# Optimization experiments

Hardware: AMD Instinct MI355X
Metric: run time of the kernel (lower is better)

Reference implementation:

```python
import jax, jax.numpy as jnp
import numpy as np

EPS = 0.01
EXPD_WEIGHT = 1.0
COMP_WEIGHT = 1.0
NUM_CLASSES = 32
M, D = 262144, 128


def setup_inputs() -> dict:
    key = jax.random.key(0)
    k1, k2 = jax.random.split(key)
    cls_score = jax.random.normal(k1, (M, D), dtype=jnp.float32)
    label = jax.random.randint(k2, (M,), 0, NUM_CLASSES)
    return {"cls_score": cls_score, "label": label}


def _logdet(X):
    sgn, ld = jnp.linalg.slogdet(X)
    return sgn * ld


def reference(cls_score, label):
    m, d = cls_score.shape
    m_f = jnp.asarray(m, cls_score.dtype)
    # expansion term: logdet(c * Z^T Z) / 2, c = d / (m * eps)
    c = d / (m_f * EPS)
    cov = cls_score.T @ cls_score  # [d, d]
    loss_expd = _logdet(c * cov) / 2.0

    # compression term: sum_j m_j/(2m) * logdet(c_j * Z_j^T Z_j)
    def per_class(j):
        mask = (label == j).astype(cls_score.dtype)  # [m]
        m_j = mask.sum()
        safe_mj = jnp.maximum(m_j, 1.0)
        c_j = d / (safe_mj * EPS)
        # Z_j^T Z_j == (mask * Z)^T Z, honoring the boolean subset without gather
        cov_j = (cls_score * mask[:, None]).T @ cls_score  # [d, d]
        ld_j = _logdet(c_j * cov_j)
        return jnp.where(m_j > 0, ld_j * m_j / (2.0 * m_f), 0.0)

    comps = jax.lax.map(per_class, jnp.arange(NUM_CLASSES))  # [J]
    loss_comp = comps.sum()

    # MCR2Loss.forward with return_all=False
    return loss_comp * COMP_WEIGHT - loss_expd * EXPD_WEIGHT
```

## Files before the change

### kernel.cpp

```cpp
#include <hip/hip_runtime.h>
#include <math.h>

#define D 128
#define NCLS 32
#define TSLOT 16
#define CHUNK 256

typedef float f32x16 __attribute__((ext_vector_type(16)));
typedef short bf16x8 __attribute__((ext_vector_type(8)));

__global__ void zero_k(int* hist) {
  int t = threadIdx.x;
  if (t < NCLS) hist[t] = 0;
}

__global__ __launch_bounds__(64) void hist_blk_k(const int* __restrict__ label, int M,
                                                 int NB, int* __restrict__ blkhist_t,
                                                 int* __restrict__ hist) {
  __shared__ int h[NCLS];
  const int lane = threadIdx.x;
  const int b = blockIdx.x;
  if (lane < NCLS) h[lane] = 0;
  __syncthreads();
  const int s0 = b * CHUNK;
#pragma unroll
  for (int it = 0; it < CHUNK / 64; ++it) {
    int i = s0 + it * 64 + lane;
    if (i < M) atomicAdd(&h[label[i]], 1);
  }
  __syncthreads();
  if (lane < NCLS) {
    blkhist_t[lane * NB + b] = h[lane];
    atomicAdd(&hist[lane], h[lane]);
  }
}

__global__ void prefix_k(const int* __restrict__ hist, int* __restrict__ cstart) {
  if (threadIdx.x == 0) {
    int run = 0;
    for (int j = 0; j < NCLS; ++j) { cstart[j] = run; run += hist[j]; }
    cstart[NCLS] = run;
  }
}

__global__ __launch_bounds__(64) void base_k(const int* __restrict__ blkhist_t,
                                             const int* __restrict__ cstart, int NB,
                                             int* __restrict__ base_t) {
  const int j = blockIdx.x;
  const int lane = threadIdx.x;
  const int K = (NB + 63) / 64;
  int vals[32];
  int run = 0;
  for (int k = 0; k < K; ++k) {
    int b = lane * K + k;
    int v = (b < NB) ? blkhist_t[j * NB + b] : 0;
    vals[k] = v;
    run += v;
  }
  int incl = run;
  for (int off = 1; off < 64; off <<= 1) {
    int o = __shfl_up(incl, off);
    if (lane >= off) incl += o;
  }
  int pos = cstart[j] + (incl - run);
  for (int k = 0; k < K; ++k) {
    int b = lane * K + k;
    if (b < NB) base_t[j * NB + b] = pos;
    pos += vals[k];
  }
}

__global__ __launch_bounds__(64) void scatter2_k(const int* __restrict__ label, int M,
                                                 int NB, const int* __restrict__ base_t,
                                                 int* __restrict__ idxbuf) {
  __shared__ int cur[NCLS];
  const int b = blockIdx.x;
  const int lane = threadIdx.x;
  if (lane < NCLS) cur[lane] = base_t[lane * NB + b];
  __syncthreads();
  const int s0 = b * CHUNK;
#pragma unroll
  for (int it = 0; it < CHUNK / 64; ++it) {
    int i = s0 + it * 64 + lane;
    int j = (i < M) ? label[i] : -1;
    unsigned long long mask = 0;
#pragma unroll
    for (int q = 0; q < NCLS; ++q) {
      unsigned long long mm = __ballot(j == q);
      if (j == q) mask = mm;
    }
    if (j >= 0) {
      int myoff = __popcll(mask & ((1ull << lane) - 1ull));
      int basec = cur[j];
      idxbuf[basec + myoff] = i;
      if (myoff == 0) cur[j] = basec + __popcll(mask);
    }
    __syncthreads();
  }
}

__device__ inline void bsplit(float x, short& hi, short& lo) {
  unsigned u = __float_as_uint(x);
  unsigned rh = u + 0x7fffu + ((u >> 16) & 1u);
  unsigned short h = (unsigned short)(rh >> 16);
  float hf = __uint_as_float((unsigned)h << 16);
  float l = x - hf;
  unsigned ul = __float_as_uint(l);
  unsigned rl = ul + 0x7fffu + ((ul >> 16) & 1u);
  hi = (short)h;
  lo = (short)(rl >> 16);
}

__global__ __launch_bounds__(512, 4) void cov_k(const float* __restrict__ Z,
                                                const int* __restrict__ idxbuf,
                                                const int* __restrict__ hist,
                                                const int* __restrict__ cstart,
                                                float* __restrict__ partials) {
  __shared__ __attribute__((aligned(16))) char arena[2 * 16896];
  char* const ThiB = arena;
  char* const TloB = arena + 16896;

  const int b = blockIdx.x;
  const int cls = b / TSLOT, slot = b % TSLOT;
  const int t = threadIdx.x;
  const int lane = t & 63;
  const int w = t >> 6;
  const int r = w >> 1;
  const int cp = (w & 1) * 2;

  const int col4 = t & 31;
  const int rg = t >> 5;
  const int wbase0 = (((rg >> 2) * 4 + (col4 >> 3)) * 2 + ((rg >> 1) & 1)) * 528 +
                     (col4 & 7) * 16 + (rg & 1) * 8;

  const int mj = hist[cls];
  const int seg0 = cstart[cls];
  const int segend = seg0 + mj;
  const int nch = (mj + 63) / 64;

  f32x16 acc[2];
#pragma unroll
  for (int u = 0; u < 2; ++u)
#pragma unroll
    for (int i = 0; i < 16; ++i) acc[u][i] = 0.f;

  const int n = lane & 31;
  const int poff = ((n >> 2) + 8 * (n & 3)) * 16 + (lane >> 5) * 528;

  float4 pv[4];
  {
    const int ch = slot;
    const int r0 = seg0 + ch * 64;
#pragma unroll
    for (int i = 0; i < 4; ++i) {
      int gr = r0 + rg * 4 + i;
      if (ch < nch && gr < segend) {
        int ridx = idxbuf[gr];
        pv[i] = *(const float4*)(Z + (size_t)ridx * D + col4 * 4);
      } else {
        pv[i] = make_float4(0.f, 0.f, 0.f, 0.f);
      }
    }
  }

  for (int ch = slot; ch < nch; ch += TSLOT) {
    __syncthreads();
    {
      float xs[4][4];
      xs[0][0] = pv[0].x; xs[0][1] = pv[0].y; xs[0][2] = pv[0].z; xs[0][3] = pv[0].w;
      xs[1][0] = pv[1].x; xs[1][1] = pv[1].y; xs[1][2] = pv[1].z; xs[1][3] = pv[1].w;
      xs[2][0] = pv[2].x; xs[2][1] = pv[2].y; xs[2][2] = pv[2].z; xs[2][3] = pv[2].w;
      xs[3][0] = pv[3].x; xs[3][1] = pv[3].y; xs[3][2] = pv[3].z; xs[3][3] = pv[3].w;
#pragma unroll
      for (int j = 0; j < 4; ++j) {
        short h0, h1, h2, h3, l0, l1, l2, l3;
        bsplit(xs[0][j], h0, l0);
        bsplit(xs[1][j], h1, l1);
        bsplit(xs[2][j], h2, l2);
        bsplit(xs[3][j], h3, l3);
        *(short4*)(ThiB + wbase0 + j * 128) = make_short4(h0, h1, h2, h3);
        *(short4*)(TloB + wbase0 + j * 128) = make_short4(l0, l1, l2, l3);
      }
    }
    __syncthreads();
    {
      const int chn = ch + TSLOT;
      const int r0 = seg0 + chn * 64;
#pragma unroll
      for (int i = 0; i < 4; ++i) {
        int gr = r0 + rg * 4 + i;
        if (chn < nch && gr < segend) {
          int ridx = idxbuf[gr];
          pv[i] = *(const float4*)(Z + (size_t)ridx * D + col4 * 4);
        } else {
          pv[i] = make_float4(0.f, 0.f, 0.f, 0.f);
        }
      }
    }
#pragma unroll
    for (int kk = 0; kk < 4; ++kk) {
      const int ab = (kk * 4 + r) * 1056 + poff;
      bf16x8 ahi = *(const bf16x8*)(ThiB + ab);
      bf16x8 alo = *(const bf16x8*)(TloB + ab);
#pragma unroll
      for (int u = 0; u < 2; ++u) {
        const int bb = (kk * 4 + cp + u) * 1056 + poff;
        bf16x8 bhi = *(const bf16x8*)(ThiB + bb);
        bf16x8 blo = *(const bf16x8*)(TloB + bb);
        acc[u] = __builtin_amdgcn_mfma_f32_32x32x16_bf16(ahi, bhi, acc[u], 0, 0, 0);
        acc[u] = __builtin_amdgcn_mfma_f32_32x32x16_bf16(ahi, blo, acc[u], 0, 0, 0);
        acc[u] = __builtin_amdgcn_mfma_f32_32x32x16_bf16(alo, bhi, acc[u], 0, 0, 0);
      }
    }
  }

  size_t base = (size_t)b * (D * D);
#pragma unroll
  for (int u = 0; u < 2; ++u)
#pragma unroll
    for (int i = 0; i < 16; ++i) {
      int prow = r * 32 + (i & 3) + 8 * (i >> 2) + 4 * (lane >> 5);
      int qcol = (cp + u) * 32 + (lane & 31);
      partials[base + (size_t)prow * D + qcol] = acc[u][i];
    }
}

__global__ void reduce_k(const float* __restrict__ partials, float* __restrict__ covs) {
  int e = blockIdx.x * blockDim.x + threadIdx.x;
  double tot = 0.0;
  for (int j = 0; j < NCLS; ++j) {
    double s = 0.0;
    for (int t = 0; t < TSLOT; ++t)
      s += (double)partials[(size_t)(j * TSLOT + t) * (D * D) + e];
    covs[(size_t)j * (D * D) + e] = (float)s;
    tot += s;
  }
  covs[(size_t)NCLS * (D * D) + e] = (float)tot;
}

__global__ __launch_bounds__(256, 1) void chol_k(const float* __restrict__ covs,
                                                 const int* __restrict__ hist,
                                                 int Mtot, double* __restrict__ results) {
  __shared__ float As[128][132];
  __shared__ float PlT[32][36];
  __shared__ float invd[32];
  __shared__ float colbuf[32];
  __shared__ double red[64];
  __shared__ __attribute__((aligned(16))) short Thi[96 * 40];
  __shared__ __attribute__((aligned(16))) short Tlo[96 * 40];
  const int j = blockIdx.x;
  const float* A = covs + (size_t)j * (D * D);
  const int tid = threadIdx.x;
  const int lane = tid & 63;
  const int wv = tid >> 6;

#pragma unroll
  for (int it = 0; it < 16; ++it) {
    int e = it * 1024 + tid * 4;
    int r = e >> 7, c = e & 127;
    *(float4*)&As[r][c] = *(const float4*)&A[e];
  }
  __syncthreads();

  double lda = 0.0;
#pragma unroll 1
  for (int p = 0; p < 4; ++p) {
    const int pbase = p * 32;
    const int N2 = 96 - pbase;
    if (wv == 0) {
      const int l = lane & 31;
      float row[32];
#pragma unroll
      for (int c4 = 0; c4 < 8; ++c4) {
        float4 v = *(const float4*)&As[pbase + l][pbase + c4 * 4];
        row[c4 * 4 + 0] = v.x; row[c4 * 4 + 1] = v.y;
        row[c4 * 4 + 2] = v.z; row[c4 * 4 + 3] = v.w;
      }
      float mypiv = 1.f, myinv = 0.f;
#pragma unroll
      for (int k = 0; k < 32; ++k) {
        colbuf[l] = row[k];
        float cb[32];
#pragma unroll
        for (int q = 0; q < 8; ++q) {
          float4 v = *(const float4*)&colbuf[q * 4];
          cb[q * 4 + 0] = v.x; cb[q * 4 + 1] = v.y;
          cb[q * 4 + 2] = v.z; cb[q * 4 + 3] = v.w;
        }
        float piv = cb[k];
        float inv = rsqrtf(piv);
        inv = inv * (1.5f - 0.5f * piv * inv * inv);
        if (lane == k) { mypiv = piv; myinv = inv; }
        float tmul = row[k] * (inv * inv);
#pragma unroll
        for (int c = k + 1; c < 32; ++c)
          row[c] = fmaf(-tmul, cb[c], row[c]);
        row[k] *= inv;
      }
      if (lane < 32) {
#pragma unroll
        for (int c = 0; c < 32; ++c) PlT[c][lane] = row[c];
        invd[lane] = myinv;
      }
      lda += log((double)mypiv);
    }
    __syncthreads();
    if (tid < N2) {
      const int R = pbase + 32 + tid;
      float s[32];
#pragma unroll
      for (int c4 = 0; c4 < 8; ++c4) {
        float4 v = *(const float4*)&As[R][pbase + c4 * 4];
        s[c4 * 4 + 0] = v.x; s[c4 * 4 + 1] = v.y;
        s[c4 * 4 + 2] = v.z; s[c4 * 4 + 3] = v.w;
      }
#pragma unroll
      for (int i = 0; i < 32; ++i) {
        float xi = s[i] * invd[i];
        s[i] = xi;
#pragma unroll
        for (int jj = i + 1; jj < 32; ++jj)
          s[jj] = fmaf(-xi, PlT[i][jj], s[jj]);
      }
      unsigned hp[16], lp[16];
#pragma unroll
      for (int q = 0; q < 16; ++q) {
        short ha, la, hb, lb;
        bsplit(s[2 * q], ha, la);
        bsplit(s[2 * q + 1], hb, lb);
        hp[q] = (unsigned)(unsigned short)ha | ((unsigned)(unsigned short)hb << 16);
        lp[q] = (unsigned)(unsigned short)la | ((unsigned)(unsigned short)lb << 16);
      }
#pragma unroll
      for (int q = 0; q < 4; ++q) {
        *(int4*)&Thi[tid * 40 + q * 8] =
            make_int4(hp[4 * q], hp[4 * q + 1], hp[4 * q + 2], hp[4 * q + 3]);
        *(int4*)&Tlo[tid * 40 + q * 8] =
            make_int4(lp[4 * q], lp[4 * q + 1], lp[4 * q + 2], lp[4 * q + 3]);
      }
    }
    __syncthreads();
    const int nstr = N2 >> 5;
    if (wv < nstr) {
      const int l31 = lane & 31;
      const int h = lane >> 5;
      const int arow = wv * 32 + l31;
#pragma unroll 1
      for (int ct = 0; ct < nstr; ++ct) {
        const int brow = ct * 32 + l31;
        f32x16 acc;
#pragma unroll
        for (int i = 0; i < 16; ++i) acc[i] = 0.f;
#pragma unroll
        for (int ks = 0; ks < 2; ++ks) {
          const int off = ks * 16 + h * 8;
          bf16x8 ahi = *(const bf16x8*)&Thi[arow * 40 + off];
          bf16x8 alo = *(const bf16x8*)&Tlo[arow * 40 + off];
          bf16x8 bhi = *(const bf16x8*)&Thi[brow * 40 + off];
          bf16x8 blo = *(const bf16x8*)&Tlo[brow * 40 + off];
          acc = __builtin_amdgcn_mfma_f32_32x32x16_bf16(ahi, bhi, acc, 0, 0, 0);
          acc = __builtin_amdgcn_mfma_f32_32x32x16_bf16(ahi, blo, acc, 0, 0, 0);
          acc = __builtin_amdgcn_mfma_f32_32x32x16_bf16(alo, bhi, acc, 0, 0, 0);
        }
#pragma unroll
        for (int i = 0; i < 16; ++i) {
          int rr = pbase + 32 + wv * 32 + (i & 3) + 8 * (i >> 2) + 4 * h;
          int cc = pbase + 32 + ct * 32 + l31;
          As[rr][cc] -= acc[i];
        }
      }
    }
    __syncthreads();
  }

  if (wv == 0) red[lane] = lda;
  __syncthreads();
  if (tid == 0) {
    double lsum = 0.0;
    for (int i = 0; i < 64; ++i) lsum += red[i];
    if (j < NCLS) {
      int mj = hist[j];
      double res = 0.0;
      if (mj > 0) {
        double cj = (double)D / ((double)mj * 0.01);
        res = ((double)D * log(cj) + lsum) * (double)mj / (2.0 * (double)Mtot);
      }
      results[j] = res;
    } else {
      double c = (double)D / ((double)Mtot * 0.01);
      results[NCLS] = ((double)D * log(c) + lsum) * 0.5;
    }
  }
}

__global__ void final_k(const double* __restrict__ results, float* __restrict__ out) {
  if (threadIdx.x == 0 && blockIdx.x == 0) {
    double s = 0.0;
    for (int j = 0; j < NCLS; ++j) s += results[j];
    out[0] = (float)(s - results[NCLS]);
  }
}

extern "C" void kernel_launch(void* const* d_in, const int* in_sizes, int n_in,
                              void* d_out, int out_size, void* d_ws, size_t ws_size,
                              hipStream_t stream) {
  const float* Z = (const float*)d_in[0];
  const int* label = (const int*)d_in[1];
  const int Mtot = in_sizes[1];
  float* out = (float*)d_out;
  const int NB = (Mtot + CHUNK - 1) / CHUNK;

  char* ws = (char*)d_ws;
  int* hist = (int*)(ws + 0);
  int* cstart = (int*)(ws + 256);
  double* results = (double*)(ws + 512);
  int* idxbuf = (int*)(ws + 1024);
  float* partials = (float*)(ws + 1024 + (size_t)Mtot * sizeof(int));
  float* covs = partials + (size_t)NCLS * TSLOT * D * D;
  int* blkhist_t = (int*)partials;
  int* base_t = blkhist_t + (size_t)NCLS * NB;

  zero_k<<<1, 64, 0, stream>>>(hist);
  hist_blk_k<<<NB, 64, 0, stream>>>(label, Mtot, NB, blkhist_t, hist);
  prefix_k<<<1, 64, 0, stream>>>(hist, cstart);
  base_k<<<NCLS, 64, 0, stream>>>(blkhist_t, cstart, NB, base_t);
  scatter2_k<<<NB, 64, 0, stream>>>(label, Mtot, NB, base_t, idxbuf);
  cov_k<<<NCLS * TSLOT, 512, 0, stream>>>(Z, idxbuf, hist, cstart, partials);
  reduce_k<<<(D * D) / 256, 256, 0, stream>>>(partials, covs);
  chol_k<<<NCLS + 1, 256, 0, stream>>>(covs, hist, Mtot, results);
  final_k<<<1, 64, 0, stream>>>(results, out);
}
```

Before: 125.1 us.

## Double cov_k block to 1024 threads and prefetch gather indices one chunk ahead

The covariance kernel now runs 16 waves per block, each owning one 32x32 output tile instead of two. Each thread stages two rows rather than four. Gather indices for the chunk after next are loaded one iteration early, so the dependent Z load no longer waits on the idxbuf read. This is meant to raise memory-level parallelism and latency hiding, at the cost of more LDS A/B fragment reads per MFMA, larger blocks and more synchronization participants. The launch_bounds occupancy hint of 8 is unlikely to be met with 1024-thread blocks.

After: 118.4 us, median of 3. 5.4% less time.

```diff
diff --git a/kernel.cpp b/kernel.cpp
--- a/kernel.cpp
+++ b/kernel.cpp
@@ -111,12 +111,12 @@
   lo = (short)(rl >> 16);
 }
 
-__global__ __launch_bounds__(512, 4) void cov_k(const float* __restrict__ Z,
-                                                const int* __restrict__ idxbuf,
-                                                const int* __restrict__ hist,
-                                                const int* __restrict__ cstart,
-                                                float* __restrict__ partials) {
-  __shared__ __attribute__((aligned(16))) char arena[2 * 16896];
+__global__ __launch_bounds__(1024, 8) void cov_k(const float* __restrict__ Z,
+                                                 const int* __restrict__ idxbuf,
+                                                 const int* __restrict__ hist,
+                                                 const int* __restrict__ cstart,
+                                                 float* __restrict__ partials) {
+  __shared__ __attribute__((aligned(16))) char arena[33792];
   char* const ThiB = arena;
   char* const TloB = arena + 16896;
 
@@ -125,104 +125,109 @@
   const int t = threadIdx.x;
   const int lane = t & 63;
   const int w = t >> 6;
-  const int r = w >> 1;
-  const int cp = (w & 1) * 2;
+  const int r = w >> 2;
+  const int cq = w & 3;
 
   const int col4 = t & 31;
   const int rg = t >> 5;
-  const int wbase0 = (((rg >> 2) * 4 + (col4 >> 3)) * 2 + ((rg >> 1) & 1)) * 528 +
-                     (col4 & 7) * 16 + (rg & 1) * 8;
+  const int wbase = (((rg >> 3) * 4 + (col4 >> 3)) * 2 + ((rg >> 2) & 1)) * 528 +
+                    (col4 & 7) * 16 + (rg & 3) * 4;
 
   const int mj = hist[cls];
   const int seg0 = cstart[cls];
   const int segend = seg0 + mj;
   const int nch = (mj + 63) / 64;
 
-  f32x16 acc[2];
-#pragma unroll
-  for (int u = 0; u < 2; ++u)
-#pragma unroll
-    for (int i = 0; i < 16; ++i) acc[u][i] = 0.f;
+  f32x16 acc;
+#pragma unroll
+  for (int i = 0; i < 16; ++i) acc[i] = 0.f;
 
   const int n = lane & 31;
   const int poff = ((n >> 2) + 8 * (n & 3)) * 16 + (lane >> 5) * 528;
 
-  float4 pv[4];
+  float4 pv[2];
+  int idxn0 = 0, idxn1 = 0;
   {
     const int ch = slot;
     const int r0 = seg0 + ch * 64;
-#pragma unroll
-    for (int i = 0; i < 4; ++i) {
-      int gr = r0 + rg * 4 + i;
-      if (ch < nch && gr < segend) {
-        int ridx = idxbuf[gr];
-        pv[i] = *(const float4*)(Z + (size_t)ridx * D + col4 * 4);
-      } else {
-        pv[i] = make_float4(0.f, 0.f, 0.f, 0.f);
-      }
-    }
-  }
-
+    int i0 = 0, i1 = 0;
+    if (ch < nch) {
+      int g0 = r0 + rg * 2, g1 = r0 + rg * 2 + 1;
+      if (g0 < segend) i0 = idxbuf[g0];
+      if (g1 < segend) i1 = idxbuf[g1];
+      pv[0] = (g0 < segend) ? *(const float4*)(Z + (size_t)i0 * D + col4 * 4)
+                            : make_float4(0.f, 0.f, 0.f, 0.f);
+      pv[1] = (g1 < segend) ? *(const float4*)(Z + (size_t)i1 * D + col4 * 4)
+                            : make_float4(0.f, 0.f, 0.f, 0.f);
+    } else {
+      pv[0] = make_float4(0.f, 0.f, 0.f, 0.f);
+      pv[1] = make_float4(0.f, 0.f, 0.f, 0.f);
+    }
+    const int chn = ch + TSLOT;
+    const int r1 = seg0 + chn * 64;
+    if (chn < nch) {
+      int g0 = r1 + rg * 2, g1 = r1 + rg * 2 + 1;
+      if (g0 < segend) idxn0 = idxbuf[g0];
+      if (g1 < segend) idxn1 = idxbuf[g1];
+    }
+  }
+
+#pragma unroll 1
   for (int ch = slot; ch < nch; ch += TSLOT) {
     __syncthreads();
     {
-      float xs[4][4];
+      float xs[2][4];
       xs[0][0] = pv[0].x; xs[0][1] = pv[0].y; xs[0][2] = pv[0].z; xs[0][3] = pv[0].w;
       xs[1][0] = pv[1].x; xs[1][1] = pv[1].y; xs[1][2] = pv[1].z; xs[1][3] = pv[1].w;
-      xs[2][0] = pv[2].x; xs[2][1] = pv[2].y; xs[2][2] = pv[2].z; xs[2][3] = pv[2].w;
-      xs[3][0] = pv[3].x; xs[3][1] = pv[3].y; xs[3][2] = pv[3].z; xs[3][3] = pv[3].w;
 #pragma unroll
       for (int j = 0; j < 4; ++j) {
-        short h0, h1, h2, h3, l0, l1, l2, l3;
+        short h0, l0, h1, l1;
         bsplit(xs[0][j], h0, l0);
         bsplit(xs[1][j], h1, l1);
-        bsplit(xs[2][j], h2, l2);
-        bsplit(xs[3][j], h3, l3);
-        *(short4*)(ThiB + wbase0 + j * 128) = make_short4(h0, h1, h2, h3);
-        *(short4*)(TloB + wbase0 + j * 128) = make_short4(l0, l1, l2, l3);
+        *(short2*)(ThiB + wbase + j * 128) = make_short2(h0, h1);
+        *(short2*)(TloB + wbase + j * 128) = make_short2(l0, l1);
       }
     }
     __syncthreads();
     {
       const int chn = ch + TSLOT;
-      const int r0 = seg0 + chn * 64;
-#pragma unroll
-      for (int i = 0; i < 4; ++i) {
-        int gr = r0 + rg * 4 + i;
-        if (chn < nch && gr < segend) {
-          int ridx = idxbuf[gr];
-          pv[i] = *(const float4*)(Z + (size_t)ridx * D + col4 * 4);
-        } else {
-          pv[i] = make_float4(0.f, 0.f, 0.f, 0.f);
-        }
+      const int r1 = seg0 + chn * 64;
+      int g0 = r1 + rg * 2, g1 = r1 + rg * 2 + 1;
+      bool v0 = (chn < nch) && (g0 < segend);
+      bool v1 = (chn < nch) && (g1 < segend);
+      pv[0] = v0 ? *(const float4*)(Z + (size_t)idxn0 * D + col4 * 4)
+                 : make_float4(0.f, 0.f, 0.f, 0.f);
+      pv[1] = v1 ? *(const float4*)(Z + (size_t)idxn1 * D + col4 * 4)
+                 : make_float4(0.f, 0.f, 0.f, 0.f);
+      const int chn2 = ch + 2 * TSLOT;
+      const int r2 = seg0 + chn2 * 64;
+      if (chn2 < nch) {
+        int h0 = r2 + rg * 2, h1 = r2 + rg * 2 + 1;
+        if (h0 < segend) idxn0 = idxbuf[h0];
+        if (h1 < segend) idxn1 = idxbuf[h1];
       }
     }
 #pragma unroll
     for (int kk = 0; kk < 4; ++kk) {
       const int ab = (kk * 4 + r) * 1056 + poff;
+      const int bb = (kk * 4 + cq) * 1056 + poff;
       bf16x8 ahi = *(const bf16x8*)(ThiB + ab);
       bf16x8 alo = *(const bf16x8*)(TloB + ab);
-#pragma unroll
-      for (int u = 0; u < 2; ++u) {
-        const int bb = (kk * 4 + cp + u) * 1056 + poff;
-        bf16x8 bhi = *(const bf16x8*)(ThiB + bb);
-        bf16x8 blo = *(const bf16x8*)(TloB + bb);
-        acc[u] = __builtin_amdgcn_mfma_f32_32x32x16_bf16(ahi, bhi, acc[u], 0, 0, 0);
-        acc[u] = __builtin_amdgcn_mfma_f32_32x32x16_bf16(ahi, blo, acc[u], 0, 0, 0);
-        acc[u] = __builtin_amdgcn_mfma_f32_32x32x16_bf16(alo, bhi, acc[u], 0, 0, 0);
-      }
+      bf16x8 bhi = *(const bf16x8*)(ThiB + bb);
+      bf16x8 blo = *(const bf16x8*)(TloB + bb);
+      acc = __builtin_amdgcn_mfma_f32_32x32x16_bf16(ahi, bhi, acc, 0, 0, 0);
+      acc = __builtin_amdgcn_mfma_f32_32x32x16_bf16(ahi, blo, acc, 0, 0, 0);
+      acc = __builtin_amdgcn_mfma_f32_32x32x16_bf16(alo, bhi, acc, 0, 0, 0);
     }
   }
 
   size_t base = (size_t)b * (D * D);
 #pragma unroll
-  for (int u = 0; u < 2; ++u)
-#pragma unroll
-    for (int i = 0; i < 16; ++i) {
-      int prow = r * 32 + (i & 3) + 8 * (i >> 2) + 4 * (lane >> 5);
-      int qcol = (cp + u) * 32 + (lane & 31);
-      partials[base + (size_t)prow * D + qcol] = acc[u][i];
-    }
+  for (int i = 0; i < 16; ++i) {
+    int prow = r * 32 + (i & 3) + 8 * (i >> 2) + 4 * (lane >> 5);
+    int qcol = cq * 32 + (lane & 31);
+    partials[base + (size_t)prow * D + qcol] = acc[i];
+  }
 }
 
 __global__ void reduce_k(const float* __restrict__ partials, float* __restrict__ covs) {
@@ -425,7 +430,7 @@
   prefix_k<<<1, 64, 0, stream>>>(hist, cstart);
   base_k<<<NCLS, 64, 0, stream>>>(blkhist_t, cstart, NB, base_t);
   scatter2_k<<<NB, 64, 0, stream>>>(label, Mtot, NB, base_t, idxbuf);
-  cov_k<<<NCLS * TSLOT, 512, 0, stream>>>(Z, idxbuf, hist, cstart, partials);
+  cov_k<<<NCLS * TSLOT, 1024, 0, stream>>>(Z, idxbuf, hist, cstart, partials);
   reduce_k<<<(D * D) / 256, 256, 0, stream>>>(partials, covs);
   chol_k<<<NCLS + 1, 256, 0, stream>>>(covs, hist, Mtot, results);
   final_k<<<1, 64, 0, stream>>>(results, out);
```

## Widen cov_k to 1024 threads with 128-row chunks and two-stage index prefetch

Applied to the files above, without the earlier changes.

The covariance kernel now uses 1024-thread blocks that stage 128 rows per chunk, doubling LDS to two 33 KB buffers. Each of the 16 waves owns a single 32x32 output tile instead of two. Row indices are prefetched two chunks ahead and out-of-range rows are zeroed with a mask instead of branches, so the gather loads become unconditional. This aims to hide gather latency and raise MFMA work per sync, at the cost of fewer resident blocks per CU and larger LDS use.

Measured after the change: 124.4 us. No clear change (-0.6%).

```diff
diff --git a/kernel.cpp b/kernel.cpp
--- a/kernel.cpp
+++ b/kernel.cpp
@@ -111,66 +111,87 @@
   lo = (short)(rl >> 16);
 }
 
-__global__ __launch_bounds__(512, 4) void cov_k(const float* __restrict__ Z,
-                                                const int* __restrict__ idxbuf,
-                                                const int* __restrict__ hist,
-                                                const int* __restrict__ cstart,
-                                                float* __restrict__ partials) {
-  __shared__ __attribute__((aligned(16))) char arena[2 * 16896];
+__global__ __launch_bounds__(1024, 8) void cov_k(const float* __restrict__ Z,
+                                                 const int* __restrict__ idxbuf,
+                                                 const int* __restrict__ hist,
+                                                 const int* __restrict__ cstart,
+                                                 float* __restrict__ partials) {
+  __shared__ __attribute__((aligned(16))) char arena[2 * 33792];
   char* const ThiB = arena;
-  char* const TloB = arena + 16896;
+  char* const TloB = arena + 33792;
 
   const int b = blockIdx.x;
   const int cls = b / TSLOT, slot = b % TSLOT;
   const int t = threadIdx.x;
   const int lane = t & 63;
   const int w = t >> 6;
-  const int r = w >> 1;
-  const int cp = (w & 1) * 2;
+  const int r = w >> 2;
+  const int cq = w & 3;
 
   const int col4 = t & 31;
   const int rg = t >> 5;
-  const int wbase0 = (((rg >> 2) * 4 + (col4 >> 3)) * 2 + ((rg >> 1) & 1)) * 528 +
-                     (col4 & 7) * 16 + (rg & 1) * 8;
+  const int wbase = ((((rg >> 2) * 4 + (col4 >> 3)) * 2 + ((rg & 3) >> 1)) * 528) +
+                    (col4 & 7) * 16 + (rg & 1) * 8;
 
   const int mj = hist[cls];
   const int seg0 = cstart[cls];
   const int segend = seg0 + mj;
-  const int nch = (mj + 63) / 64;
-
-  f32x16 acc[2];
-#pragma unroll
-  for (int u = 0; u < 2; ++u)
-#pragma unroll
-    for (int i = 0; i < 16; ++i) acc[u][i] = 0.f;
+  const int nch = (mj + 127) / 128;
+
+  f32x16 acc;
+#pragma unroll
+  for (int i = 0; i < 16; ++i) acc[i] = 0.f;
 
   const int n = lane & 31;
   const int poff = ((n >> 2) + 8 * (n & 3)) * 16 + (lane >> 5) * 528;
 
   float4 pv[4];
-  {
-    const int ch = slot;
-    const int r0 = seg0 + ch * 64;
+  float msk[4];
+  int idxn[4];
+
+  if (mj > 0) {
+    const int ch0 = slot;
+    if (ch0 < nch) {
+      const int r0 = seg0 + ch0 * 128;
+      int ii[4];
+#pragma unroll
+      for (int i = 0; i < 4; ++i) {
+        int g = r0 + rg * 4 + i;
+        bool v = g < segend;
+        msk[i] = v ? 1.f : 0.f;
+        ii[i] = idxbuf[v ? g : seg0];
+      }
+#pragma unroll
+      for (int i = 0; i < 4; ++i)
+        pv[i] = *(const float4*)(Z + (size_t)ii[i] * D + col4 * 4);
+    } else {
+#pragma unroll
+      for (int i = 0; i < 4; ++i) {
+        msk[i] = 0.f;
+        pv[i] = make_float4(0.f, 0.f, 0.f, 0.f);
+      }
+    }
+    const int ch1 = slot + TSLOT;
+    const int r1 = seg0 + ch1 * 128;
 #pragma unroll
     for (int i = 0; i < 4; ++i) {
-      int gr = r0 + rg * 4 + i;
-      if (ch < nch && gr < segend) {
-        int ridx = idxbuf[gr];
-        pv[i] = *(const float4*)(Z + (size_t)ridx * D + col4 * 4);
-      } else {
-        pv[i] = make_float4(0.f, 0.f, 0.f, 0.f);
-      }
-    }
-  }
-
+      int g = r1 + rg * 4 + i;
+      idxn[i] = idxbuf[(ch1 < nch && g < segend) ? g : seg0];
+    }
+  }
+
+#pragma unroll 1
   for (int ch = slot; ch < nch; ch += TSLOT) {
     __syncthreads();
     {
       float xs[4][4];
-      xs[0][0] = pv[0].x; xs[0][1] = pv[0].y; xs[0][2] = pv[0].z; xs[0][3] = pv[0].w;
-      xs[1][0] = pv[1].x; xs[1][1] = pv[1].y; xs[1][2] = pv[1].z; xs[1][3] = pv[1].w;
-      xs[2][0] = pv[2].x; xs[2][1] = pv[2].y; xs[2][2] = pv[2].z; xs[2][3] = pv[2].w;
-      xs[3][0] = pv[3].x; xs[3][1] = pv[3].y; xs[3][2] = pv[3].z; xs[3][3] = pv[3].w;
+#pragma unroll
+      for (int i = 0; i < 4; ++i) {
+        xs[i][0] = pv[i].x * msk[i];
+        xs[i][1] = pv[i].y * msk[i];
+        xs[i][2] = pv[i].z * msk[i];
+        xs[i][3] = pv[i].w * msk[i];
+      }
 #pragma unroll
       for (int j = 0; j < 4; ++j) {
         short h0, h1, h2, h3, l0, l1, l2, l3;
@@ -178,51 +199,51 @@
         bsplit(xs[1][j], h1, l1);
         bsplit(xs[2][j], h2, l2);
         bsplit(xs[3][j], h3, l3);
-        *(short4*)(ThiB + wbase0 + j * 128) = make_short4(h0, h1, h2, h3);
-        *(short4*)(TloB + wbase0 + j * 128) = make_short4(l0, l1, l2, l3);
+        *(short4*)(ThiB + wbase + j * 128) = make_short4(h0, h1, h2, h3);
+        *(short4*)(TloB + wbase + j * 128) = make_short4(l0, l1, l2, l3);
       }
     }
     __syncthreads();
     {
       const int chn = ch + TSLOT;
-      const int r0 = seg0 + chn * 64;
+      const int rn = seg0 + chn * 128;
 #pragma unroll
       for (int i = 0; i < 4; ++i) {
-        int gr = r0 + rg * 4 + i;
-        if (chn < nch && gr < segend) {
-          int ridx = idxbuf[gr];
-          pv[i] = *(const float4*)(Z + (size_t)ridx * D + col4 * 4);
-        } else {
-          pv[i] = make_float4(0.f, 0.f, 0.f, 0.f);
-        }
-      }
-    }
-#pragma unroll
-    for (int kk = 0; kk < 4; ++kk) {
+        int g = rn + rg * 4 + i;
+        msk[i] = (chn < nch && g < segend) ? 1.f : 0.f;
+      }
+#pragma unroll
+      for (int i = 0; i < 4; ++i)
+        pv[i] = *(const float4*)(Z + (size_t)idxn[i] * D + col4 * 4);
+      const int chn2 = ch + 2 * TSLOT;
+      const int r2 = seg0 + chn2 * 128;
+#pragma unroll
+      for (int i = 0; i < 4; ++i) {
+        int g = r2 + rg * 4 + i;
+        idxn[i] = idxbuf[(chn2 < nch && g < segend) ? g : seg0];
+      }
+    }
+#pragma unroll
+    for (int kk = 0; kk < 8; ++kk) {
       const int ab = (kk * 4 + r) * 1056 + poff;
+      const int bb = (kk * 4 + cq) * 1056 + poff;
       bf16x8 ahi = *(const bf16x8*)(ThiB + ab);
       bf16x8 alo = *(const bf16x8*)(TloB + ab);
-#pragma unroll
-      for (int u = 0; u < 2; ++u) {
-        const int bb = (kk * 4 + cp + u) * 1056 + poff;
-        bf16x8 bhi = *(const bf16x8*)(ThiB + bb);
-        bf16x8 blo = *(const bf16x8*)(TloB + bb);
-        acc[u] = __builtin_amdgcn_mfma_f32_32x32x16_bf16(ahi, bhi, acc[u], 0, 0, 0);
-        acc[u] = __builtin_amdgcn_mfma_f32_32x32x16_bf16(ahi, blo, acc[u], 0, 0, 0);
-        acc[u] = __builtin_amdgcn_mfma_f32_32x32x16_bf16(alo, bhi, acc[u], 0, 0, 0);
-      }
+      bf16x8 bhi = *(const bf16x8*)(ThiB + bb);
+      bf16x8 blo = *(const bf16x8*)(TloB + bb);
+      acc = __builtin_amdgcn_mfma_f32_32x32x16_bf16(ahi, bhi, acc, 0, 0, 0);
+      acc = __builtin_amdgcn_mfma_f32_32x32x16_bf16(ahi, blo, acc, 0, 0, 0);
+      acc = __builtin_amdgcn_mfma_f32_32x32x16_bf16(alo, bhi, acc, 0, 0, 0);
     }
   }
 
   size_t base = (size_t)b * (D * D);
 #pragma unroll
-  for (int u = 0; u < 2; ++u)
-#pragma unroll
-    for (int i = 0; i < 16; ++i) {
-      int prow = r * 32 + (i & 3) + 8 * (i >> 2) + 4 * (lane >> 5);
-      int qcol = (cp + u) * 32 + (lane & 31);
-      partials[base + (size_t)prow * D + qcol] = acc[u][i];
-    }
+  for (int i = 0; i < 16; ++i) {
+    int prow = r * 32 + (i & 3) + 8 * (i >> 2) + 4 * (lane >> 5);
+    int qcol = cq * 32 + (lane & 31);
+    partials[base + (size_t)prow * D + qcol] = acc[i];
+  }
 }
 
 __global__ void reduce_k(const float* __restrict__ partials, float* __restrict__ covs) {
@@ -425,7 +446,7 @@
   prefix_k<<<1, 64, 0, stream>>>(hist, cstart);
   base_k<<<NCLS, 64, 0, stream>>>(blkhist_t, cstart, NB, base_t);
   scatter2_k<<<NB, 64, 0, stream>>>(label, Mtot, NB, base_t, idxbuf);
-  cov_k<<<NCLS * TSLOT, 512, 0, stream>>>(Z, idxbuf, hist, cstart, partials);
+  cov_k<<<NCLS * TSLOT, 1024, 0, stream>>>(Z, idxbuf, hist, cstart, partials);
   reduce_k<<<(D * D) / 256, 256, 0, stream>>>(partials, covs);
   chol_k<<<NCLS + 1, 256, 0, stream>>>(covs, hist, Mtot, results);
   final_k<<<1, 64, 0, stream>>>(results, out);
```
